# Optimization experiments

Hardware: AMD Instinct MI355X
Metric: run time of the kernel (lower is better)

## Reference

```python
import jax, jax.numpy as jnp
import numpy as np

N, F_IN, F_OUT = 8192, 512, 256
NEG_BIG = -9e15


def setup_inputs() -> dict:
    key = jax.random.key(0)
    k1, k2, k3, k4, k5 = jax.random.split(key, 5)
    h = jax.random.normal(k1, (N, F_IN), dtype=jnp.float32)
    adj = jax.random.randint(k2, (N, N), 0, 2, dtype=jnp.int32)
    W = jax.random.normal(k3, (F_IN, F_OUT), dtype=jnp.float32) / np.sqrt(F_IN)
    bW = jnp.zeros((F_OUT,), dtype=jnp.float32)
    a1 = jax.random.normal(k4, (F_OUT,), dtype=jnp.float32) / np.sqrt(2 * F_OUT)
    a2 = jax.random.normal(k5, (F_OUT,), dtype=jnp.float32) / np.sqrt(2 * F_OUT)
    ba = jnp.zeros((), dtype=jnp.float32)
    return {"h": h, "adj": adj, "W": W, "bW": bW, "a1": a1, "a2": a2, "ba": ba}


def reference(h, adj, W, bW, a1, a2, ba):
    # Wh: [N, F_OUT]
    Wh = h @ W + bW
    # a([Wh_i ; Wh_j]) + b == (Wh_i . a1) + (Wh_j . a2) + b  (rank-1 decomposition,
    # avoids the O(N^2 * 2F) repeat/cat tensor the torch code materializes)
    f1 = Wh @ a1  # [N]
    f2 = Wh @ a2  # [N]
    e = jax.nn.leaky_relu(f1[:, None] + f2[None, :] + ba, negative_slope=0.2)
    e = jnp.where(adj > 0, e, NEG_BIG)
    attention = jax.nn.softmax(e, axis=1)  # dropout = identity (eval mode)
    return attention @ Wh
```

## Files before the change

kernel.cpp:

```cpp
#include <hip/hip_runtime.h>

typedef __bf16 bf16;
typedef __attribute__((ext_vector_type(4))) float f32x4;
typedef __attribute__((ext_vector_type(8))) __bf16 bf16x8;
typedef __attribute__((ext_vector_type(4))) __bf16 bf16x4;
typedef __attribute__((ext_vector_type(4))) int i32x4;

#define NN 8192
#define FI 512
#define FO 256
#define NSPLIT 8
#define JCHUNK (NN / NSPLIT)
#define KSTEPS (JCHUNK / 32)

__global__ __launch_bounds__(256) void kw_split(const float* __restrict__ W,
                                                bf16* __restrict__ wth,
                                                bf16* __restrict__ wtl) {
  const int idx = blockIdx.x * 256 + threadIdx.x;
  const int k = idx >> 8, n = idx & 255;
  float x = W[idx];
  bf16 hi = (bf16)x;
  wth[(size_t)n * FI + k] = hi;
  wtl[(size_t)n * FI + k] = (bf16)(x - (float)hi);
}

__global__ __launch_bounds__(256) void k1_gemm(
    const float* __restrict__ h, const bf16* __restrict__ wth,
    const bf16* __restrict__ wtl, const float* __restrict__ bW,
    const float* __restrict__ a1, const float* __restrict__ a2,
    bf16* __restrict__ whb, float* __restrict__ f1, float* __restrict__ f2) {
  __shared__ bf16 Ah[32 * 40];
  __shared__ bf16 Al[32 * 40];
  const int t = threadIdx.x;
  const int lane = t & 63, w = t >> 6;
  const int m16 = lane & 15, q = lane >> 4;
  const int bi = blockIdx.x, bj = blockIdx.y;
  const int i0 = bi * 32;
  const int n0 = bj * 128 + w * 32;
  const int srow = t >> 3, skoff = (t & 7) * 4;

  const f32x4 z4 = {0.f, 0.f, 0.f, 0.f};
  f32x4 acc[2][2];
#pragma unroll
  for (int mt = 0; mt < 2; ++mt)
#pragma unroll
    for (int nt = 0; nt < 2; ++nt) acc[mt][nt] = z4;

  const float* hrow = h + (size_t)(i0 + srow) * FI + skoff;

  for (int kt = 0; kt < FI / 32; ++kt) {
    f32x4 hv = *(const f32x4*)(hrow + kt * 32);
    bf16x8 bh[2], bl[2];
#pragma unroll
    for (int nt = 0; nt < 2; ++nt) {
      const size_t woff = (size_t)(n0 + nt * 16 + m16) * FI + kt * 32 + q * 8;
      bh[nt] = *(const bf16x8*)(wth + woff);
      bl[nt] = *(const bf16x8*)(wtl + woff);
    }
    bf16x4 hh, hl;
#pragma unroll
    for (int x = 0; x < 4; ++x) {
      float v = hv[x];
      bf16 hi = (bf16)v;
      hh[x] = hi;
      hl[x] = (bf16)(v - (float)hi);
    }
    __syncthreads();
    *(bf16x4*)&Ah[srow * 40 + skoff] = hh;
    *(bf16x4*)&Al[srow * 40 + skoff] = hl;
    __syncthreads();
#pragma unroll
    for (int mt = 0; mt < 2; ++mt) {
      bf16x8 ah = *(const bf16x8*)&Ah[(mt * 16 + m16) * 40 + q * 8];
      bf16x8 al = *(const bf16x8*)&Al[(mt * 16 + m16) * 40 + q * 8];
#pragma unroll
      for (int nt = 0; nt < 2; ++nt) {
        acc[mt][nt] = __builtin_amdgcn_mfma_f32_16x16x32_bf16(ah, bh[nt], acc[mt][nt], 0, 0, 0);
        acc[mt][nt] = __builtin_amdgcn_mfma_f32_16x16x32_bf16(al, bh[nt], acc[mt][nt], 0, 0, 0);
        acc[mt][nt] = __builtin_amdgcn_mfma_f32_16x16x32_bf16(ah, bl[nt], acc[mt][nt], 0, 0, 0);
      }
    }
  }
  float f1p[2][4] = {}, f2p[2][4] = {};
#pragma unroll
  for (int nt = 0; nt < 2; ++nt) {
    const int n = n0 + nt * 16 + m16;
    const float bw = bW[n], av1 = a1[n], av2 = a2[n];
#pragma unroll
    for (int mt = 0; mt < 2; ++mt) {
#pragma unroll
      for (int reg = 0; reg < 4; ++reg) {
        float wh = acc[mt][nt][reg] + bw;
        const int il = mt * 16 + q * 4 + reg;
        whb[(size_t)bi * (FO * 32) + n * 32 + il] = (bf16)wh;
        f1p[mt][reg] += wh * av1;
        f2p[mt][reg] += wh * av2;
      }
    }
  }
#pragma unroll
  for (int m = 1; m < 16; m <<= 1) {
#pragma unroll
    for (int mt = 0; mt < 2; ++mt)
#pragma unroll
      for (int reg = 0; reg < 4; ++reg) {
        f1p[mt][reg] += __shfl_xor(f1p[mt][reg], m);
        f2p[mt][reg] += __shfl_xor(f2p[mt][reg], m);
      }
  }
  if (m16 == 0) {
#pragma unroll
    for (int mt = 0; mt < 2; ++mt)
#pragma unroll
      for (int reg = 0; reg < 4; ++reg) {
        const int i = i0 + mt * 16 + q * 4 + reg;
        atomicAdd(&f1[i], f1p[mt][reg]);
        atomicAdd(&f2[i], f2p[mt][reg]);
      }
  }
}

__global__ __launch_bounds__(256) void k3_max(const float* __restrict__ f2,
                                              float* __restrict__ Mstar) {
  __shared__ float red[4];
  const int t = threadIdx.x;
  float m = -1e30f;
  for (int i = t; i < NN; i += 256) m = fmaxf(m, f2[i]);
#pragma unroll
  for (int d = 1; d < 64; d <<= 1) m = fmaxf(m, __shfl_xor(m, d));
  if ((t & 63) == 0) red[t >> 6] = m;
  __syncthreads();
  if (t == 0) *Mstar = fmaxf(fmaxf(red[0], red[1]), fmaxf(red[2], red[3]));
}

__global__ __launch_bounds__(256, 2) void k4_attn(
    const int* __restrict__ adj, const bf16* __restrict__ whb,
    const float* __restrict__ f1, const float* __restrict__ f2,
    const float* __restrict__ Mstar, const float* __restrict__ ba_p,
    float* __restrict__ acc_part, float* __restrict__ l_part) {
  const int t = threadIdx.x;
  const int lane = t & 63, w = t >> 6;
  const int m16 = lane & 15, q = lane >> 4;
  const int rb = blockIdx.x, s = blockIdx.y;
  const int i0 = rb * 64;
  const int jq = q * 8;

  const float ba = *ba_p;
  const float Ms = *Mstar;
  float ci[4], sh[4];
  const int* arow[4];
#pragma unroll
  for (int rt = 0; rt < 4; ++rt) {
    const int r = i0 + rt * 16 + m16;
    ci[rt] = f1[r] + ba;
    float v = ci[rt] + Ms;
    sh[rt] = fmaxf(v, 0.2f * v);
    arow[rt] = adj + (size_t)r * NN;
  }

  const f32x4 z4 = {0.f, 0.f, 0.f, 0.f};
  f32x4 acc[4][4];
#pragma unroll
  for (int rt = 0; rt < 4; ++rt)
#pragma unroll
    for (int cc = 0; cc < 4; ++cc) acc[rt][cc] = z4;
  float lreg[4] = {0.f, 0.f, 0.f, 0.f};

  const int sbase = s * JCHUNK;

  i32x4 a0[4], a1r[4];
  f32x4 fa0, fa1;
#pragma unroll
  for (int rt = 0; rt < 4; ++rt) {
    a0[rt] = *(const i32x4*)(arow[rt] + sbase + jq);
    a1r[rt] = *(const i32x4*)(arow[rt] + sbase + jq + 4);
  }
  fa0 = *(const f32x4*)(f2 + sbase + jq);
  fa1 = *(const f32x4*)(f2 + sbase + jq + 4);

  for (int kt = 0; kt < KSTEPS; ++kt) {
    const int j0 = sbase + kt * 32;

    bf16x8 bfr[4];
    const size_t bbase = (size_t)(j0 >> 5) * (FO * 32) + jq;
#pragma unroll
    for (int cc = 0; cc < 4; ++cc)
      bfr[cc] = *(const bf16x8*)(whb + bbase + (size_t)((w * 4 + cc) * 16 + m16) * 32);

    const int ktn = (kt + 1 < KSTEPS) ? kt + 1 : kt;
    const int j0n = sbase + ktn * 32;
    i32x4 a0n[4], a1n[4];
#pragma unroll
    for (int rt = 0; rt < 4; ++rt) {
      a0n[rt] = *(const i32x4*)(arow[rt] + j0n + jq);
      a1n[rt] = *(const i32x4*)(arow[rt] + j0n + jq + 4);
    }
    f32x4 fa0n = *(const f32x4*)(f2 + j0n + jq);
    f32x4 fa1n = *(const f32x4*)(f2 + j0n + jq + 4);

    bf16x8 af[4];
#pragma unroll
    for (int rt = 0; rt < 4; ++rt) {
      float pv[8];
#pragma unroll
      for (int x = 0; x < 4; ++x) {
        float arg = ci[rt] + fa0[x];
        float e = fmaxf(arg, 0.2f * arg);
        pv[x] = (a0[rt][x] > 0) ? __expf(e - sh[rt]) : 0.f;
      }
#pragma unroll
      for (int x = 0; x < 4; ++x) {
        float arg = ci[rt] + fa1[x];
        float e = fmaxf(arg, 0.2f * arg);
        pv[4 + x] = (a1r[rt][x] > 0) ? __expf(e - sh[rt]) : 0.f;
      }
#pragma unroll
      for (int x = 0; x < 8; ++x) lreg[rt] += pv[x];
#pragma unroll
      for (int x = 0; x < 8; ++x) af[rt][x] = (bf16)pv[x];
    }

#pragma unroll
    for (int rt = 0; rt < 4; ++rt)
#pragma unroll
      for (int cc = 0; cc < 4; ++cc)
        acc[rt][cc] = __builtin_amdgcn_mfma_f32_16x16x32_bf16(af[rt], bfr[cc], acc[rt][cc], 0, 0, 0);

#pragma unroll
    for (int rt = 0; rt < 4; ++rt) { a0[rt] = a0n[rt]; a1r[rt] = a1n[rt]; }
    fa0 = fa0n; fa1 = fa1n;
  }

#pragma unroll
  for (int rt = 0; rt < 4; ++rt) {
    float lr = lreg[rt];
    lr += __shfl_xor(lr, 16);
    lr += __shfl_xor(lr, 32);
    if (q == 0) l_part[(size_t)s * NN + i0 + rt * 16 + m16] = lr;
  }
  float* ap = acc_part + (size_t)s * ((size_t)NN * FO);
#pragma unroll
  for (int rt = 0; rt < 4; ++rt) {
#pragma unroll
    for (int cc = 0; cc < 4; ++cc) {
      const int n = (w * 4 + cc) * 16 + m16;
#pragma unroll
      for (int reg = 0; reg < 4; ++reg) {
        const int r = i0 + rt * 16 + q * 4 + reg;
        ap[(size_t)r * FO + n] = acc[rt][cc][reg];
      }
    }
  }
}

__global__ __launch_bounds__(256) void k5_reduce(
    const float* __restrict__ accp, const float* __restrict__ lp,
    float* __restrict__ out) {
  const int idx = blockIdx.x * 256 + threadIdx.x;
  const int i = idx >> 6, n4 = (idx & 63) * 4;
  f32x4 sum = {0.f, 0.f, 0.f, 0.f};
  float l = 0.f;
#pragma unroll
  for (int s = 0; s < NSPLIT; ++s) {
    sum += *(const f32x4*)&accp[(size_t)s * ((size_t)NN * FO) + (size_t)i * FO + n4];
    l += lp[s * NN + i];
  }
  const float rl = 1.0f / l;
  f32x4 o = sum * rl;
  *(f32x4*)&out[(size_t)i * FO + n4] = o;
}

extern "C" void kernel_launch(void* const* d_in, const int* in_sizes, int n_in,
                              void* d_out, int out_size, void* d_ws, size_t ws_size,
                              hipStream_t stream) {
  const float* h   = (const float*)d_in[0];
  const int*   adj = (const int*)d_in[1];
  const float* W   = (const float*)d_in[2];
  const float* bW  = (const float*)d_in[3];
  const float* a1  = (const float*)d_in[4];
  const float* a2  = (const float*)d_in[5];
  const float* ba  = (const float*)d_in[6];
  float* out = (float*)d_out;

  char* ws = (char*)d_ws;
  bf16* whb   = (bf16*)ws;
  float* f1   = (float*)(ws + 4u * 1024 * 1024);
  float* f2   = (float*)(ws + 4u * 1024 * 1024 + 32 * 1024);
  float* Mst  = (float*)(ws + 4u * 1024 * 1024 + 64 * 1024);
  float* accp = (float*)(ws + 4u * 1024 * 1024 + 64 * 1024 + 256);
  float* lp   = accp + (size_t)NSPLIT * NN * FO;
  bf16* wth   = (bf16*)((char*)lp + (size_t)NSPLIT * NN * 4);
  bf16* wtl   = wth + (size_t)FO * FI;

  hipMemsetAsync(f1, 0, 64 * 1024, stream);

  kw_split<<<FI * FO / 256, 256, 0, stream>>>(W, wth, wtl);
  k1_gemm<<<dim3(NN / 32, 2), 256, 0, stream>>>(h, wth, wtl, bW, a1, a2, whb, f1, f2);
  k3_max<<<1, 256, 0, stream>>>(f2, Mst);
  k4_attn<<<dim3(NN / 64, NSPLIT), 256, 0, stream>>>(adj, whb, f1, f2, Mst, ba, accp, lp);
  k5_reduce<<<(NN * FO / 4) / 256, 256, 0, stream>>>(accp, lp, out);
}
```

Measured before the change: 517.0 us.

## Pack adjacency into bitmask, use exp2 with prescaled logits, retile attention waves

A new pre-pass packs the int32 adjacency matrix into one bit per edge, and the attention kernel reads these bytes instead of re-reading the int32 rows. f2 and the row constants are prescaled by log2(e), so the softmax numerator uses a raw exp2 with the LeakyReLU folded into one fma/max. Each wave now owns 2 row tiles by 8 column tiles instead of 4 by 4. That halves the exp/mask work per wave, since the mask and exp values were previously recomputed by every column-owning wave, but it doubles the B-fragment loads. The pack pass still reads the full 256 MB adjacency once and adds an extra launch.

```diff
diff --git a/kernel.cpp b/kernel.cpp
--- a/kernel.cpp
+++ b/kernel.cpp
@@ -12,6 +12,20 @@
 #define NSPLIT 8
 #define JCHUNK (NN / NSPLIT)
 #define KSTEPS (JCHUNK / 32)
+#define LOG2E 1.4426950408889634f
+
+__global__ __launch_bounds__(256) void k0_pack(const int* __restrict__ adj,
+                                               unsigned char* __restrict__ maskb) {
+  const size_t gid = (size_t)blockIdx.x * 256 + threadIdx.x;
+  const int* p = adj + gid * 8;
+  i32x4 v0 = *(const i32x4*)(p);
+  i32x4 v1 = *(const i32x4*)(p + 4);
+  unsigned m = (unsigned)(v0.x > 0) | ((unsigned)(v0.y > 0) << 1) |
+               ((unsigned)(v0.z > 0) << 2) | ((unsigned)(v0.w > 0) << 3) |
+               ((unsigned)(v1.x > 0) << 4) | ((unsigned)(v1.y > 0) << 5) |
+               ((unsigned)(v1.z > 0) << 6) | ((unsigned)(v1.w > 0) << 7);
+  maskb[gid] = (unsigned char)m;
+}
 
 __global__ __launch_bounds__(256) void kw_split(const float* __restrict__ W,
                                                 bf16* __restrict__ wth,
@@ -121,11 +135,16 @@
 }
 
 __global__ __launch_bounds__(256) void k3_max(const float* __restrict__ f2,
+                                              float* __restrict__ f2L,
                                               float* __restrict__ Mstar) {
   __shared__ float red[4];
   const int t = threadIdx.x;
   float m = -1e30f;
-  for (int i = t; i < NN; i += 256) m = fmaxf(m, f2[i]);
+  for (int i = t; i < NN; i += 256) {
+    float v = f2[i];
+    f2L[i] = v * LOG2E;
+    m = fmaxf(m, v);
+  }
 #pragma unroll
   for (int d = 1; d < 64; d <<= 1) m = fmaxf(m, __shfl_xor(m, d));
   if ((t & 63) == 0) red[t >> 6] = m;
@@ -134,8 +153,8 @@
 }
 
 __global__ __launch_bounds__(256, 2) void k4_attn(
-    const int* __restrict__ adj, const bf16* __restrict__ whb,
-    const float* __restrict__ f1, const float* __restrict__ f2,
+    const unsigned char* __restrict__ maskb, const bf16* __restrict__ whb,
+    const float* __restrict__ f1, const float* __restrict__ f2L,
     const float* __restrict__ Mstar, const float* __restrict__ ba_p,
     float* __restrict__ acc_part, float* __restrict__ l_part) {
   const int t = threadIdx.x;
@@ -144,75 +163,76 @@
   const int rb = blockIdx.x, s = blockIdx.y;
   const int i0 = rb * 64;
   const int jq = q * 8;
+  const int wr = w & 1;
+  const int wc = w >> 1;
 
   const float ba = *ba_p;
   const float Ms = *Mstar;
-  float ci[4], sh[4];
-  const int* arow[4];
-#pragma unroll
-  for (int rt = 0; rt < 4; ++rt) {
-    const int r = i0 + rt * 16 + m16;
-    ci[rt] = f1[r] + ba;
-    float v = ci[rt] + Ms;
-    sh[rt] = fmaxf(v, 0.2f * v);
-    arow[rt] = adj + (size_t)r * NN;
+  float ciLs[2], c2[2];
+  const unsigned char* mrow[2];
+#pragma unroll
+  for (int rt = 0; rt < 2; ++rt) {
+    const int r = i0 + wr * 32 + rt * 16 + m16;
+    float ci = f1[r] + ba;
+    float v = ci + Ms;
+    float sh = fmaxf(v, 0.2f * v);
+    float shl = sh * LOG2E;
+    ciLs[rt] = ci * LOG2E - shl;
+    c2[rt] = -0.8f * shl;
+    mrow[rt] = maskb + ((size_t)r << 10);
   }
 
   const f32x4 z4 = {0.f, 0.f, 0.f, 0.f};
-  f32x4 acc[4][4];
-#pragma unroll
-  for (int rt = 0; rt < 4; ++rt)
-#pragma unroll
-    for (int cc = 0; cc < 4; ++cc) acc[rt][cc] = z4;
-  float lreg[4] = {0.f, 0.f, 0.f, 0.f};
+  f32x4 acc[2][8];
+#pragma unroll
+  for (int rt = 0; rt < 2; ++rt)
+#pragma unroll
+    for (int cc = 0; cc < 8; ++cc) acc[rt][cc] = z4;
+  float lreg[2] = {0.f, 0.f};
 
   const int sbase = s * JCHUNK;
 
-  i32x4 a0[4], a1r[4];
-  f32x4 fa0, fa1;
-#pragma unroll
-  for (int rt = 0; rt < 4; ++rt) {
-    a0[rt] = *(const i32x4*)(arow[rt] + sbase + jq);
-    a1r[rt] = *(const i32x4*)(arow[rt] + sbase + jq + 4);
-  }
-  fa0 = *(const f32x4*)(f2 + sbase + jq);
-  fa1 = *(const f32x4*)(f2 + sbase + jq + 4);
+  int mcur[2];
+#pragma unroll
+  for (int rt = 0; rt < 2; ++rt) mcur[rt] = mrow[rt][(sbase >> 3) + q];
+  f32x4 fa0 = *(const f32x4*)(f2L + sbase + jq);
+  f32x4 fa1 = *(const f32x4*)(f2L + sbase + jq + 4);
 
   for (int kt = 0; kt < KSTEPS; ++kt) {
     const int j0 = sbase + kt * 32;
 
-    bf16x8 bfr[4];
+    bf16x8 bfr[8];
     const size_t bbase = (size_t)(j0 >> 5) * (FO * 32) + jq;
 #pragma unroll
-    for (int cc = 0; cc < 4; ++cc)
-      bfr[cc] = *(const bf16x8*)(whb + bbase + (size_t)((w * 4 + cc) * 16 + m16) * 32);
+    for (int cc = 0; cc < 8; ++cc)
+      bfr[cc] = *(const bf16x8*)(whb + bbase + (size_t)((wc * 8 + cc) * 16 + m16) * 32);
 
     const int ktn = (kt + 1 < KSTEPS) ? kt + 1 : kt;
     const int j0n = sbase + ktn * 32;
-    i32x4 a0n[4], a1n[4];
-#pragma unroll
-    for (int rt = 0; rt < 4; ++rt) {
-      a0n[rt] = *(const i32x4*)(arow[rt] + j0n + jq);
-      a1n[rt] = *(const i32x4*)(arow[rt] + j0n + jq + 4);
-    }
-    f32x4 fa0n = *(const f32x4*)(f2 + j0n + jq);
-    f32x4 fa1n = *(const f32x4*)(f2 + j0n + jq + 4);
-
-    bf16x8 af[4];
-#pragma unroll
-    for (int rt = 0; rt < 4; ++rt) {
+    int mnx[2];
+#pragma unroll
+    for (int rt = 0; rt < 2; ++rt) mnx[rt] = mrow[rt][(j0n >> 3) + q];
+    f32x4 fa0n = *(const f32x4*)(f2L + j0n + jq);
+    f32x4 fa1n = *(const f32x4*)(f2L + j0n + jq + 4);
+
+    bf16x8 af[2];
+#pragma unroll
+    for (int rt = 0; rt < 2; ++rt) {
+      const int mb = mcur[rt];
       float pv[8];
 #pragma unroll
       for (int x = 0; x < 4; ++x) {
-        float arg = ci[rt] + fa0[x];
-        float e = fmaxf(arg, 0.2f * arg);
-        pv[x] = (a0[rt][x] > 0) ? __expf(e - sh[rt]) : 0.f;
-      }
-#pragma unroll
-      for (int x = 0; x < 4; ++x) {
-        float arg = ci[rt] + fa1[x];
-        float e = fmaxf(arg, 0.2f * arg);
-        pv[4 + x] = (a1r[rt][x] > 0) ? __expf(e - sh[rt]) : 0.f;
+        float A = ciLs[rt] + fa0[x];
+        float e2 = fmaxf(A, fmaf(0.2f, A, c2[rt]));
+        float val = __builtin_amdgcn_exp2f(e2);
+        pv[x] = ((mb >> x) & 1) ? val : 0.f;
+      }
+#pragma unroll
+      for (int x = 4; x < 8; ++x) {
+        float A = ciLs[rt] + fa1[x - 4];
+        float e2 = fmaxf(A, fmaf(0.2f, A, c2[rt]));
+        float val = __builtin_amdgcn_exp2f(e2);
+        pv[x] = ((mb >> x) & 1) ? val : 0.f;
       }
 #pragma unroll
       for (int x = 0; x < 8; ++x) lreg[rt] += pv[x];
@@ -221,32 +241,32 @@
     }
 
 #pragma unroll
-    for (int rt = 0; rt < 4; ++rt)
-#pragma unroll
-      for (int cc = 0; cc < 4; ++cc)
+    for (int rt = 0; rt < 2; ++rt)
+#pragma unroll
+      for (int cc = 0; cc < 8; ++cc)
         acc[rt][cc] = __builtin_amdgcn_mfma_f32_16x16x32_bf16(af[rt], bfr[cc], acc[rt][cc], 0, 0, 0);
 
-#pragma unroll
-    for (int rt = 0; rt < 4; ++rt) { a0[rt] = a0n[rt]; a1r[rt] = a1n[rt]; }
+    mcur[0] = mnx[0]; mcur[1] = mnx[1];
     fa0 = fa0n; fa1 = fa1n;
   }
 
 #pragma unroll
-  for (int rt = 0; rt < 4; ++rt) {
+  for (int rt = 0; rt < 2; ++rt) {
     float lr = lreg[rt];
     lr += __shfl_xor(lr, 16);
     lr += __shfl_xor(lr, 32);
-    if (q == 0) l_part[(size_t)s * NN + i0 + rt * 16 + m16] = lr;
+    if (wc == 0 && q == 0)
+      l_part[(size_t)s * NN + i0 + wr * 32 + rt * 16 + m16] = lr;
   }
   float* ap = acc_part + (size_t)s * ((size_t)NN * FO);
 #pragma unroll
-  for (int rt = 0; rt < 4; ++rt) {
-#pragma unroll
-    for (int cc = 0; cc < 4; ++cc) {
-      const int n = (w * 4 + cc) * 16 + m16;
+  for (int rt = 0; rt < 2; ++rt) {
+#pragma unroll
+    for (int cc = 0; cc < 8; ++cc) {
+      const int n = (wc * 8 + cc) * 16 + m16;
 #pragma unroll
       for (int reg = 0; reg < 4; ++reg) {
-        const int r = i0 + rt * 16 + q * 4 + reg;
+        const int r = i0 + wr * 32 + rt * 16 + q * 4 + reg;
         ap[(size_t)r * FO + n] = acc[rt][cc][reg];
       }
     }
@@ -286,17 +306,20 @@
   bf16* whb   = (bf16*)ws;
   float* f1   = (float*)(ws + 4u * 1024 * 1024);
   float* f2   = (float*)(ws + 4u * 1024 * 1024 + 32 * 1024);
-  float* Mst  = (float*)(ws + 4u * 1024 * 1024 + 64 * 1024);
-  float* accp = (float*)(ws + 4u * 1024 * 1024 + 64 * 1024 + 256);
+  float* f2L  = (float*)(ws + 4u * 1024 * 1024 + 64 * 1024);
+  float* Mst  = (float*)(ws + 4u * 1024 * 1024 + 96 * 1024);
+  float* accp = (float*)(ws + 4u * 1024 * 1024 + 96 * 1024 + 256);
   float* lp   = accp + (size_t)NSPLIT * NN * FO;
-  bf16* wth   = (bf16*)((char*)lp + (size_t)NSPLIT * NN * 4);
+  unsigned char* maskb = (unsigned char*)((char*)lp + (size_t)NSPLIT * NN * 4);
+  bf16* wth   = (bf16*)((char*)maskb + (size_t)NN * (NN / 8));
   bf16* wtl   = wth + (size_t)FO * FI;
 
   hipMemsetAsync(f1, 0, 64 * 1024, stream);
 
+  k0_pack<<<NN * NN / 8 / 256, 256, 0, stream>>>(adj, maskb);
   kw_split<<<FI * FO / 256, 256, 0, stream>>>(W, wth, wtl);
   k1_gemm<<<dim3(NN / 32, 2), 256, 0, stream>>>(h, wth, wtl, bW, a1, a2, whb, f1, f2);
-  k3_max<<<1, 256, 0, stream>>>(f2, Mst);
-  k4_attn<<<dim3(NN / 64, NSPLIT), 256, 0, stream>>>(adj, whb, f1, f2, Mst, ba, accp, lp);
+  k3_max<<<1, 256, 0, stream>>>(f2, f2L, Mst);
+  k4_attn<<<dim3(NN / 64, NSPLIT), 256, 0, stream>>>(maskb, whb, f1, f2L, Mst, ba, accp, lp);
   k5_reduce<<<(NN * FO / 4) / 256, 256, 0, stream>>>(accp, lp, out);
 }
```

Measured after the change: 541.4 us. 4.7% more time.
